# Kernel optimization log

Hardware: AMD Instinct MI355X
Metric: run time of the kernel (lower is better)

Reference implementation:

```python
import jax, jax.numpy as jnp
import numpy as np

N = 100000
E = 1600000
IN_C, HID_C, OUT_C = 128, 128, 64


def setup_inputs() -> dict:
    key = jax.random.key(0)
    ks = jax.random.split(key, 8)
    x = jax.random.normal(ks[0], (N, IN_C), dtype=jnp.float32)
    edge_index = jax.random.randint(ks[1], (2, E), 0, N, dtype=jnp.int64)

    def glorot(k, fan_in, fan_out):
        s = jnp.sqrt(6.0 / (fan_in + fan_out))
        return jax.random.uniform(k, (fan_in, fan_out), jnp.float32, -s, s)

    W1 = glorot(ks[2], IN_C, HID_C)
    b1 = jnp.zeros((HID_C,), jnp.float32)
    W2 = glorot(ks[3], HID_C, HID_C)
    b2 = jnp.zeros((HID_C,), jnp.float32)
    W3 = glorot(ks[4], HID_C, OUT_C)
    b3 = jnp.zeros((OUT_C,), jnp.float32)
    return {"x": x, "edge_index": edge_index,
            "W1": W1, "b1": b1, "W2": W2, "b2": b2, "W3": W3, "b3": b3}


def _gcn_norm(row, col, n_nodes):
    # symmetric normalization, add_self_loops=False (PyG gcn_norm)
    deg = jax.ops.segment_sum(jnp.ones(row.shape[0], jnp.float32), col, num_segments=n_nodes)
    dinv = jnp.where(deg > 0, jax.lax.rsqrt(jnp.maximum(deg, 1.0)), 0.0)
    dinv = jnp.where(deg > 0, deg ** -0.5, 0.0)
    return dinv[row] * dinv[col]  # [E]


def _gcn_conv(x, row, col, norm, W, b):
    h = x @ W                                # [N, F_out] dense GEMM first (PyG order)
    msg = h[row] * norm[:, None]             # gather + scale, [E, F_out]
    out = jax.ops.segment_sum(msg, col, num_segments=x.shape[0])  # scatter-add
    return out + b


def reference(x, edge_index, W1, b1, W2, b2, W3, b3):
    row, col = edge_index[0], edge_index[1]
    norm = _gcn_norm(row, col, x.shape[0])
    h = jax.nn.relu(_gcn_conv(x, row, col, norm, W1, b1))   # dropout is identity in eval
    h = jax.nn.relu(_gcn_conv(h, row, col, norm, W2, b2))
    out = _gcn_conv(h, row, col, norm, W3, b3)
    return out
```

## Files before the change

### kernel.cpp

```cpp
#include <hip/hip_runtime.h>
#include <hip/hip_bf16.h>
#include <hip/hip_fp16.h>


#define K_DIM 128
#define SCAN_CHUNK 1024

typedef _Float16 f16x8 __attribute__((ext_vector_type(8)));
typedef float f32x4 __attribute__((ext_vector_type(4)));
typedef const __attribute__((address_space(1))) void gbl_void;
typedef __attribute__((address_space(3))) void lds_void;
struct h2s { _Float16 x, y; };

static inline long long cdiv_ll(long long a, long long b) { return (a + b - 1) / b; }

__global__ __launch_bounds__(256) void count_kernel(const int* __restrict__ col, int* __restrict__ cnt,
                                                    int* __restrict__ rank, int E) {
    int e = blockIdx.x * 256 + threadIdx.x;
    if (e < E) rank[e] = atomicAdd(&cnt[col[e]], 1);
}

__global__ __launch_bounds__(256) void dinv_kernel(const int* __restrict__ cnt, float* __restrict__ dinv, int N) {
    int n = blockIdx.x * 256 + threadIdx.x;
    if (n < N) {
        int d = cnt[n];
        dinv[n] = (d > 0) ? (1.0f / sqrtf((float)d)) : 0.0f;
    }
}

__global__ __launch_bounds__(256) void scan1_kernel(const int* __restrict__ cnt, int* __restrict__ off,
                                                    int* __restrict__ bsum, int N) {
    __shared__ int lds[256];
    const int t = threadIdx.x;
    const int base = blockIdx.x * SCAN_CHUNK;
    int v[4], s = 0;
#pragma unroll
    for (int j = 0; j < 4; ++j) {
        int i = base + t * 4 + j;
        v[j] = (i < N) ? cnt[i] : 0;
        s += v[j];
    }
    lds[t] = s;
    __syncthreads();
    for (int d = 1; d < 256; d <<= 1) {
        int x = (t >= d) ? lds[t - d] : 0;
        __syncthreads();
        lds[t] += x;
        __syncthreads();
    }
    int excl = lds[t] - s;
    if (t == 255) bsum[blockIdx.x] = lds[255];
    int run = excl;
#pragma unroll
    for (int j = 0; j < 4; ++j) {
        int i = base + t * 4 + j;
        if (i < N) off[i] = run;
        run += v[j];
    }
}

__global__ __launch_bounds__(256) void scan2_kernel(int* __restrict__ bsum, int G, int* __restrict__ off,
                                                    int N, int E) {
    __shared__ int lds[256];
    const int t = threadIdx.x;
    int s = (t < G) ? bsum[t] : 0;
    lds[t] = s;
    __syncthreads();
    for (int d = 1; d < 256; d <<= 1) {
        int x = (t >= d) ? lds[t - d] : 0;
        __syncthreads();
        lds[t] += x;
        __syncthreads();
    }
    if (t < G) bsum[t] = lds[t] - s;
    if (t == 0) off[N] = E;
}

__global__ __launch_bounds__(256) void scan3_kernel(int* __restrict__ off, const int* __restrict__ bsum, int N) {
    int add = bsum[blockIdx.x];
    const int base = blockIdx.x * SCAN_CHUNK;
#pragma unroll
    for (int j = 0; j < 4; ++j) {
        int i = base + threadIdx.x * 4 + j;
        if (i < N) off[i] += add;
    }
}

__global__ __launch_bounds__(256) void fill_kernel(const int* __restrict__ row, const int* __restrict__ col,
                                                   const int* __restrict__ off, const int* __restrict__ rank,
                                                   int* __restrict__ csr_row, int E) {
    int e = blockIdx.x * 256 + threadIdx.x;
    if (e < E) {
        int idx = off[col[e]] + rank[e];
        __builtin_nontemporal_store(row[e], &csr_row[idx]);
    }
}

template <int COUT>
__global__ __launch_bounds__(256) void pack_w_kernel(const float* __restrict__ W, _Float16* __restrict__ Wp) {
    constexpr int NT = COUT / 16;
    int t = blockIdx.x * 256 + threadIdx.x;
    if (t >= 4 * NT * 64) return;
    int lane = t & 63;
    int nt = (t >> 6) % NT;
    int kt = t / (64 * NT);
    int c = lane & 15, q = lane >> 4;
    f16x8 v;
#pragma unroll
    for (int j = 0; j < 8; ++j) {
        int k = kt * 32 + q * 8 + j;
        v[j] = (_Float16)W[k * COUT + nt * 16 + c];
    }
    *(f16x8*)&Wp[(size_t)t * 8] = v;
}

template <int COUT, bool AF16>
__global__ __launch_bounds__(256) void gemm_mfma(const void* __restrict__ Av, const _Float16* __restrict__ Wp,
                                                 const float* __restrict__ dinv, _Float16* __restrict__ Cmat, int M) {
    constexpr int NT = COUT / 16;
    constexpr int NFRAG = 4 * NT * 64;
    __shared__ _Float16 Wlds[NFRAG * 8];

    const int t = threadIdx.x;
    for (int i = t; i < NFRAG; i += 256)
        *(f16x8*)&Wlds[(size_t)i * 8] = *(const f16x8*)&Wp[(size_t)i * 8];
    __syncthreads();

    const int lane = t & 63;
    const int wave = t >> 6;
    const int c = lane & 15;
    const int q = lane >> 4;
    const int row_base = blockIdx.x * 128 + wave * 32;

    f32x4 acc[2][NT];
#pragma unroll
    for (int rt = 0; rt < 2; ++rt)
#pragma unroll
        for (int nt = 0; nt < NT; ++nt) {
            acc[rt][nt][0] = 0.f; acc[rt][nt][1] = 0.f;
            acc[rt][nt][2] = 0.f; acc[rt][nt][3] = 0.f;
        }

#pragma unroll
    for (int kt = 0; kt < 4; ++kt) {
        f16x8 a[2];
#pragma unroll
        for (int rt = 0; rt < 2; ++rt) {
            int r = row_base + rt * 16 + c;
            r = (r < M) ? r : (M - 1);
            if (AF16) {
                const _Float16* Ap = (const _Float16*)Av;
                int p = kt * 2 + (q >> 1);
                a[rt] = *(const f16x8*)&Ap[((size_t)p * M + r) * 16 + (q & 1) * 8];
            } else {
                const float* ap = (const float*)Av + (size_t)r * K_DIM + kt * 32 + q * 8;
                float4 v0 = *(const float4*)ap;
                float4 v1 = *(const float4*)(ap + 4);
                f16x8 av;
                av[0] = (_Float16)v0.x; av[1] = (_Float16)v0.y;
                av[2] = (_Float16)v0.z; av[3] = (_Float16)v0.w;
                av[4] = (_Float16)v1.x; av[5] = (_Float16)v1.y;
                av[6] = (_Float16)v1.z; av[7] = (_Float16)v1.w;
                a[rt] = av;
            }
        }
#pragma unroll
        for (int nt = 0; nt < NT; ++nt) {
            f16x8 b = *(const f16x8*)&Wlds[(size_t)((kt * NT + nt) * 64 + lane) * 8];
            acc[0][nt] = __builtin_amdgcn_mfma_f32_16x16x32_f16(a[0], b, acc[0][nt], 0, 0, 0);
            acc[1][nt] = __builtin_amdgcn_mfma_f32_16x16x32_f16(a[1], b, acc[1][nt], 0, 0, 0);
        }
    }

#pragma unroll
    for (int rt = 0; rt < 2; ++rt)
#pragma unroll
        for (int reg = 0; reg < 4; ++reg) {
            int row = row_base + rt * 16 + q * 4 + reg;
            if (row < M) {
                float dv = dinv[row];
#pragma unroll
                for (int nt = 0; nt < NT; ++nt)
                    Cmat[((size_t)nt * M + row) * 16 + c] = (_Float16)(acc[rt][nt][reg] * dv);
            }
        }
}

template <int NP, bool RELU, typename OutT>
__global__ __launch_bounds__(256) void gather_pl(const _Float16* __restrict__ g, const int* __restrict__ off,
                                                 const int* __restrict__ csr_row, const float* __restrict__ dinv,
                                                 const float* __restrict__ bias, OutT* __restrict__ outp, int N) {
    constexpr int NTILE = 128;
    constexpr int CH = 512;
    __shared__ _Float16 feat[CH * 16];
    __shared__ int off_s[NTILE + 1];

    const int t = threadIdx.x;
    const int plane = blockIdx.x % NP;
    const int node0 = (blockIdx.x / NP) * NTILE;
    const _Float16* gp = g + (size_t)plane * N * 16;

    if (t <= NTILE) {
        int idx = node0 + t;
        off_s[t] = off[idx < N ? idx : N];
    }
    __syncthreads();

    const int h = t & 1;
    const int n_loc = t >> 1;
    const int w = t >> 6;
    const int l = t & 63;
    const int node = node0 + n_loc;
    const bool valid = node < N;
    const int sn0 = off_s[n_loc];
    const int sn1 = off_s[n_loc + 1];
    const int s_begin = off_s[0];
    const int s_end = off_s[NTILE];

    float acc[8];
#pragma unroll
    for (int k = 0; k < 8; ++k) acc[k] = 0.f;

    for (int cs = s_begin; cs < s_end; cs += CH) {
        const int ce = (cs + CH < s_end) ? (cs + CH) : s_end;
        const int cnt = ce - cs;
        const int kmax = (cnt + 127) >> 7;
        for (int k = 0; k < kmax; ++k) {
            int i = k * 128 + w * 32 + (l >> 1);
            if (i < cnt) {
                int r = csr_row[cs + i];
                const _Float16* src = gp + (size_t)r * 16 + (l & 1) * 8;
                __builtin_amdgcn_global_load_lds((gbl_void*)src,
                                                 (lds_void*)&feat[((size_t)k * 128 + w * 32) * 16],
                                                 16, 0, 0);
            }
        }
        __syncthreads();
        const int lo_s = (sn0 > cs) ? sn0 : cs;
        const int hi_s = (sn1 < ce) ? sn1 : ce;
        for (int s = lo_s; s < hi_s; ++s) {
            f16x8 v = *(const f16x8*)&feat[(size_t)(s - cs) * 16 + h * 8];
#pragma unroll
            for (int k = 0; k < 8; ++k) acc[k] += (float)v[k];
        }
        __syncthreads();
    }

    if (valid) {
        float dv = dinv[node];
        float o[8];
#pragma unroll
        for (int k = 0; k < 8; ++k) {
            o[k] = acc[k] * dv + bias[plane * 16 + h * 8 + k];
            if (RELU) o[k] = fmaxf(o[k], 0.f);
        }
        if constexpr (sizeof(OutT) == 2) {
            f16x8 hv;
#pragma unroll
            for (int k = 0; k < 8; ++k) hv[k] = (_Float16)o[k];
            *(f16x8*)((_Float16*)outp + ((size_t)plane * N + node) * 16 + h * 8) = hv;
        } else {
            float* op = (float*)outp + (size_t)node * 64 + plane * 16 + h * 8;
            *(float4*)op = make_float4(o[0], o[1], o[2], o[3]);
            *(float4*)(op + 4) = make_float4(o[4], o[5], o[6], o[7]);
        }
    }
}

extern "C" void kernel_launch(void* const* d_in, const int* in_sizes, int n_in,
                              void* d_out, int out_size, void* d_ws, size_t ws_size,
                              hipStream_t stream) {
    const float* x  = (const float*)d_in[0];
    const int*   ei = (const int*)d_in[1];
    const float* W1 = (const float*)d_in[2];
    const float* b1 = (const float*)d_in[3];
    const float* W2 = (const float*)d_in[4];
    const float* b2 = (const float*)d_in[5];
    const float* W3 = (const float*)d_in[6];
    const float* b3 = (const float*)d_in[7];

    const int N = in_sizes[0] / 128;
    const int E = in_sizes[1] / 2;
    const int* row = ei;
    const int* col = ei + E;
    const int G = (int)cdiv_ll(N, SCAN_CHUNK);

    char* wsb = (char*)d_ws;
    int*      cnt     = (int*)wsb;      wsb += (size_t)N * 4;
    float*    dinv    = (float*)wsb;    wsb += (size_t)N * 4;
    int*      off     = (int*)wsb;      wsb += (size_t)(N + 1) * 4;
    int*      bsum    = (int*)wsb;      wsb += 256 * 4;
    int*      rank    = (int*)wsb;      wsb += (size_t)E * 4;
    int*      csr_row = (int*)wsb;      wsb += (size_t)E * 4;
    wsb = (char*)((((uintptr_t)wsb) + 255) & ~(uintptr_t)255);
    _Float16* Wp1     = (_Float16*)wsb; wsb += 16384 * 2;
    _Float16* Wp2     = (_Float16*)wsb; wsb += 16384 * 2;
    _Float16* Wp3     = (_Float16*)wsb; wsb += 8192 * 2;
    _Float16* bufA    = (_Float16*)wsb; wsb += (size_t)N * 128 * 2;
    _Float16* bufB    = (_Float16*)wsb;
    float*    out     = (float*)d_out;

    hipMemsetAsync(cnt, 0, (size_t)N * 4, stream);
    count_kernel<<<cdiv_ll(E, 256), 256, 0, stream>>>(col, cnt, rank, E);
    dinv_kernel<<<cdiv_ll(N, 256), 256, 0, stream>>>(cnt, dinv, N);
    scan1_kernel<<<G, 256, 0, stream>>>(cnt, off, bsum, N);
    scan2_kernel<<<1, 256, 0, stream>>>(bsum, G, off, N, E);
    scan3_kernel<<<G, 256, 0, stream>>>(off, bsum, N);
    fill_kernel<<<cdiv_ll(E, 256), 256, 0, stream>>>(row, col, off, rank, csr_row, E);
    pack_w_kernel<128><<<8, 256, 0, stream>>>(W1, Wp1);
    pack_w_kernel<128><<<8, 256, 0, stream>>>(W2, Wp2);
    pack_w_kernel<64><<<4, 256, 0, stream>>>(W3, Wp3);

    const long long gemmBlocks = cdiv_ll(N, 128);
    const long long nb         = cdiv_ll(N, 128);

    gemm_mfma<128, false><<<gemmBlocks, 256, 0, stream>>>(x, Wp1, dinv, bufA, N);
    gather_pl<8, true, _Float16><<<nb * 8, 256, 0, stream>>>(bufA, off, csr_row, dinv, b1, bufB, N);

    gemm_mfma<128, true><<<gemmBlocks, 256, 0, stream>>>(bufB, Wp2, dinv, bufA, N);
    gather_pl<8, true, _Float16><<<nb * 8, 256, 0, stream>>>(bufA, off, csr_row, dinv, b2, bufB, N);

    gemm_mfma<64, true><<<gemmBlocks, 256, 0, stream>>>(bufB, Wp3, dinv, bufA, N);
    gather_pl<4, false, float><<<nb * 4, 256, 0, stream>>>(bufA, off, csr_row, dinv, b3, out, N);
}
```

Baseline: 483.3 us.

## Double-buffer LDS feature chunks and prefetch CSR indices in gather kernel

The gather/aggregate kernel now keeps two LDS feature buffers. While the current 512-edge chunk is being summed, the async global-to-LDS loads for the next chunk are already in flight. CSR row indices for the chunk after that are prefetched into registers, so the index load no longer sits on the critical path before each feature gather. This trades twice the LDS footprint per block, which may lower occupancy, for overlap of gather latency with accumulation.

Result: slower. 522.0 us (+8.0%).

```diff
diff --git a/kernel.cpp b/kernel.cpp
--- a/kernel.cpp
+++ b/kernel.cpp
@@ -187,12 +187,12 @@
 }
 
 template <int NP, bool RELU, typename OutT>
-__global__ __launch_bounds__(256) void gather_pl(const _Float16* __restrict__ g, const int* __restrict__ off,
+__global__ __launch_bounds__(256) void gather_db(const _Float16* __restrict__ g, const int* __restrict__ off,
                                                  const int* __restrict__ csr_row, const float* __restrict__ dinv,
                                                  const float* __restrict__ bias, OutT* __restrict__ outp, int N) {
     constexpr int NTILE = 128;
     constexpr int CH = 512;
-    __shared__ _Float16 feat[CH * 16];
+    __shared__ _Float16 feat[2][CH * 16];
     __shared__ int off_s[NTILE + 1];
 
     const int t = threadIdx.x;
@@ -216,34 +216,76 @@
     const int sn1 = off_s[n_loc + 1];
     const int s_begin = off_s[0];
     const int s_end = off_s[NTILE];
+    const int nch = (s_end - s_begin + CH - 1) / CH;
+
+    const int slot = w * 32 + (l >> 1);
 
     float acc[8];
 #pragma unroll
     for (int k = 0; k < 8; ++k) acc[k] = 0.f;
 
-    for (int cs = s_begin; cs < s_end; cs += CH) {
-        const int ce = (cs + CH < s_end) ? (cs + CH) : s_end;
-        const int cnt = ce - cs;
-        const int kmax = (cnt + 127) >> 7;
-        for (int k = 0; k < kmax; ++k) {
-            int i = k * 128 + w * 32 + (l >> 1);
-            if (i < cnt) {
-                int r = csr_row[cs + i];
-                const _Float16* src = gp + (size_t)r * 16 + (l & 1) * 8;
-                __builtin_amdgcn_global_load_lds((gbl_void*)src,
-                                                 (lds_void*)&feat[((size_t)k * 128 + w * 32) * 16],
-                                                 16, 0, 0);
-            }
-        }
-        __syncthreads();
-        const int lo_s = (sn0 > cs) ? sn0 : cs;
-        const int hi_s = (sn1 < ce) ? sn1 : ce;
-        for (int s = lo_s; s < hi_s; ++s) {
-            f16x8 v = *(const f16x8*)&feat[(size_t)(s - cs) * 16 + h * 8];
-#pragma unroll
-            for (int k = 0; k < 8; ++k) acc[k] += (float)v[k];
-        }
-        __syncthreads();
+    if (nch > 0) {
+        int csrv[4];
+#pragma unroll
+        for (int k = 0; k < 4; ++k) {
+            int idx = s_begin + k * 128 + slot;
+            csrv[k] = csr_row[idx < s_end ? idx : s_end - 1];
+        }
+        {
+            const int cnt = (s_end - s_begin < CH) ? (s_end - s_begin) : CH;
+#pragma unroll
+            for (int k = 0; k < 4; ++k) {
+                if (k * 128 + slot < cnt) {
+                    const _Float16* src = gp + (size_t)csrv[k] * 16 + (l & 1) * 8;
+                    __builtin_amdgcn_global_load_lds((gbl_void*)src,
+                                                     (lds_void*)&feat[0][(size_t)(k * 128 + w * 32) * 16],
+                                                     16, 0, 0);
+                }
+            }
+        }
+        if (nch > 1) {
+#pragma unroll
+            for (int k = 0; k < 4; ++k) {
+                int idx = s_begin + CH + k * 128 + slot;
+                csrv[k] = csr_row[idx < s_end ? idx : s_end - 1];
+            }
+        }
+        __syncthreads();
+
+        for (int c = 0; c < nch; ++c) {
+            const int cs = s_begin + c * CH;
+            const int ce = (cs + CH < s_end) ? (cs + CH) : s_end;
+            if (c + 1 < nch) {
+                const int cs1 = cs + CH;
+                const int cnt1 = (s_end - cs1 < CH) ? (s_end - cs1) : CH;
+#pragma unroll
+                for (int k = 0; k < 4; ++k) {
+                    if (k * 128 + slot < cnt1) {
+                        const _Float16* src = gp + (size_t)csrv[k] * 16 + (l & 1) * 8;
+                        __builtin_amdgcn_global_load_lds((gbl_void*)src,
+                                                         (lds_void*)&feat[(c + 1) & 1][(size_t)(k * 128 + w * 32) * 16],
+                                                         16, 0, 0);
+                    }
+                }
+                if (c + 2 < nch) {
+                    const int cs2 = cs + 2 * CH;
+#pragma unroll
+                    for (int k = 0; k < 4; ++k) {
+                        int idx = cs2 + k * 128 + slot;
+                        csrv[k] = csr_row[idx < s_end ? idx : s_end - 1];
+                    }
+                }
+            }
+            const int lo_s = (sn0 > cs) ? sn0 : cs;
+            const int hi_s = (sn1 < ce) ? sn1 : ce;
+            const _Float16* fb = &feat[c & 1][0];
+            for (int s = lo_s; s < hi_s; ++s) {
+                f16x8 v = *(const f16x8*)&fb[(size_t)(s - cs) * 16 + h * 8];
+#pragma unroll
+                for (int k = 0; k < 8; ++k) acc[k] += (float)v[k];
+            }
+            __syncthreads();
+        }
     }
 
     if (valid) {
@@ -315,11 +357,11 @@
     const long long nb         = cdiv_ll(N, 128);
 
     gemm_mfma<128, false><<<gemmBlocks, 256, 0, stream>>>(x, Wp1, dinv, bufA, N);
-    gather_pl<8, true, _Float16><<<nb * 8, 256, 0, stream>>>(bufA, off, csr_row, dinv, b1, bufB, N);
+    gather_db<8, true, _Float16><<<nb * 8, 256, 0, stream>>>(bufA, off, csr_row, dinv, b1, bufB, N);
 
     gemm_mfma<128, true><<<gemmBlocks, 256, 0, stream>>>(bufB, Wp2, dinv, bufA, N);
-    gather_pl<8, true, _Float16><<<nb * 8, 256, 0, stream>>>(bufA, off, csr_row, dinv, b2, bufB, N);
+    gather_db<8, true, _Float16><<<nb * 8, 256, 0, stream>>>(bufA, off, csr_row, dinv, b2, bufB, N);
 
     gemm_mfma<64, true><<<gemmBlocks, 256, 0, stream>>>(bufB, Wp3, dinv, bufA, N);
-    gather_pl<4, false, float><<<nb * 4, 256, 0, stream>>>(bufA, off, csr_row, dinv, b3, out, N);
-}
+    gather_db<4, false, float><<<nb * 4, 256, 0, stream>>>(bufA, off, csr_row, dinv, b3, out, N);
+}
```
